# Optimization experiments

Measured on AMD Instinct MI355X. Metric: run time of the kernel, lower is better.

The kernel has to match this reference:

```python
import jax, jax.numpy as jnp
import numpy as np

ODE_UNFOLDS = 6
MOTOR_SIZE = 3
EPS = 1e-8

def _conv(x, w, b, stride):
    y = jax.lax.conv_general_dilated(x, w, (stride, stride), 'VALID',
                                     dimension_numbers=('NCHW', 'OIHW', 'NCHW'))
    return jax.nn.relu(y + b[None, :, None, None])

def _conv_head(x, w1, b1, w2, b2, w3, b3, w4, b4, w5, b5, fc_w, fc_b):
    # x: [B, T, 3, 66, 200] -> features [B, T, 128]
    B, T = x.shape[0], x.shape[1]
    h = x.reshape(B * T, *x.shape[2:])
    h = _conv(h, w1, b1, 2)  # [BT,24,31,98]
    h = _conv(h, w2, b2, 2)  # [BT,36,14,47]
    h = _conv(h, w3, b3, 2)  # [BT,48,5,22]
    h = _conv(h, w4, b4, 1)  # [BT,64,3,20]
    h = _conv(h, w5, b5, 1)  # [BT,64,1,18]
    h = h.reshape(B * T, -1)
    h = jax.nn.relu(h @ fc_w + fc_b)
    return h.reshape(B, T, -1)

def _ltc_step(inputs, v, s_mu, s_sigma, s_w, s_erev, mu, sigma, w, erev, gleak, vleak, cm):
    # inputs: [B,S], v: [B,N]
    # sensory synapse activations (constant over the ODE unfolds)
    s_act = s_w * jax.nn.sigmoid((inputs[:, :, None] - s_mu) * s_sigma)  # [B,S,N]
    w_num_s = jnp.sum(s_act * s_erev, axis=1)  # [B,N]
    w_den_s = jnp.sum(s_act, axis=1)           # [B,N]
    cm_t = cm * ODE_UNFOLDS  # cm / (elapsed=1 / ode_unfolds)
    for _ in range(ODE_UNFOLDS):
        w_act = w * jax.nn.sigmoid((v[:, :, None] - mu) * sigma)  # [B,N,N]
        w_num = jnp.sum(w_act * erev, axis=1) + w_num_s
        w_den = jnp.sum(w_act, axis=1) + w_den_s
        v = (cm_t * v + gleak * vleak + w_num) / (cm_t + gleak + w_den + EPS)
    return v[:, :MOTOR_SIZE], v

def reference(x, w1, b1, w2, b2, w3, b3, w4, b4, w5, b5, fc_w, fc_b,
              s_mu, s_sigma, s_w, s_erev, mu, sigma, w, erev, gleak, vleak, cm):
    y = _conv_head(x, w1, b1, w2, b2, w3, b3, w4, b4, w5, b5, fc_w, fc_b)  # [B,T,128]
    B, T, _ = y.shape
    N = mu.shape[0]
    v0 = jnp.zeros((B, N), dtype=y.dtype)

    def step(v, inp):
        out, v = _ltc_step(inp, v, s_mu, s_sigma, s_w, s_erev, mu, sigma, w, erev, gleak, vleak, cm)
        return v, out

    _, outs = jax.lax.scan(step, v0, jnp.swapaxes(y, 0, 1))  # outs: [T,B,3]
    return jnp.swapaxes(outs, 0, 1)  # [B,T,3]

def setup_inputs() -> dict:
    key = jax.random.key(0)
    ks = jax.random.split(key, 24)
    d = {}
    d['x'] = jax.random.normal(ks[0], (32, 16, 3, 66, 200), jnp.float32)
    shapes = [((24, 3, 5, 5), (24,)), ((36, 24, 5, 5), (36,)), ((48, 36, 5, 5), (48,)),
              ((64, 48, 3, 3), (64,)), ((64, 64, 3, 3), (64,))]
    for i, (ws, bs) in enumerate(shapes):
        d[f'w{i+1}'] = jax.random.normal(ks[1 + i], ws, jnp.float32) * 0.05
        d[f'b{i+1}'] = jnp.zeros(bs, jnp.float32)
    d['fc_w'] = jax.random.normal(ks[6], (1152, 128), jnp.float32) * 0.05
    d['fc_b'] = jnp.zeros((128,), jnp.float32)
    S, N = 128, 64
    d['s_mu'] = jax.random.normal(ks[7], (S, N), jnp.float32) * 0.3 + 0.3
    d['s_sigma'] = jax.random.uniform(ks[8], (S, N), jnp.float32, 3.0, 8.0)
    d['s_w'] = jax.random.uniform(ks[9], (S, N), jnp.float32, 0.001, 1.0)
    d['s_erev'] = jnp.sign(jax.random.normal(ks[10], (S, N), jnp.float32))
    d['mu'] = jax.random.normal(ks[11], (N, N), jnp.float32) * 0.3 + 0.3
    d['sigma'] = jax.random.uniform(ks[12], (N, N), jnp.float32, 3.0, 8.0)
    d['w'] = jax.random.uniform(ks[13], (N, N), jnp.float32, 0.001, 1.0)
    d['erev'] = jnp.sign(jax.random.normal(ks[14], (N, N), jnp.float32))
    d['gleak'] = jax.random.uniform(ks[15], (N,), jnp.float32, 0.001, 1.0)
    d['vleak'] = jax.random.uniform(ks[16], (N,), jnp.float32, -0.2, 0.2)
    d['cm'] = jax.random.uniform(ks[17], (N,), jnp.float32, 0.4, 0.6)
    return d
```

## Files before the change

### kernel.cpp

```cpp
#include <hip/hip_runtime.h>
#include <hip/hip_bf16.h>


typedef _Float16 f16;
typedef _Float16 f16x8 __attribute__((ext_vector_type(8)));
typedef _Float16 f16x4 __attribute__((ext_vector_type(4)));
typedef float    f32x4 __attribute__((ext_vector_type(4)));
typedef unsigned int u32;

static __device__ __forceinline__ float sigmoidf_fast(float x) {
    return __builtin_amdgcn_rcpf(1.0f + __expf(-x));
}

static __device__ __forceinline__ void gload_lds16(const void* g, void* l) {
    __builtin_amdgcn_global_load_lds(
        (const __attribute__((address_space(1))) void*)g,
        (__attribute__((address_space(3))) void*)l, 16, 0, 0);
}


__global__ __launch_bounds__(256)
void wpack1_kernel(const float* __restrict__ w1, f16* __restrict__ Wpk1)
{
    int idx = blockIdx.x * 256 + threadIdx.x;
    if (idx >= 32 * 136) return;
    int co = idx / 136;
    int kk = idx % 136;
    float v = 0.0f;
    if (co < 24 && kk < 120) {
        int p = kk >> 3, jj = kk & 7;
        int kh = p / 3, kwp = p % 3;
        int kws = jj >> 2, ci = jj & 3;
        int kw = 2 * kwp + kws;
        if (kw < 5 && ci < 3)
            v = w1[(((size_t)co * 3 + ci) * 5 + kh) * 5 + kw];
    }
    Wpk1[idx] = (f16)v;
}

__global__ __launch_bounds__(512)
void conv1_mfma(const float* __restrict__ x, const f16* __restrict__ Wpk1,
                const float* __restrict__ b1, f16* __restrict__ h1T)
{
    __shared__ __align__(16) f16 img[35 * 200 * 4];

    int blk  = blockIdx.x;
    int m    = blk >> 1;
    int hf   = blk & 1;
    int tid  = threadIdx.x;
    int lane = tid & 63;
    int wv   = tid >> 6;
    int col  = lane & 15;
    int row4 = lane >> 4;

    int ho_base = hf * 16;
    int r0      = 2 * ho_base;
    int nrows   = hf ? 33 : 35;
    int nho     = hf ? 15 : 16;
    int npx     = nho * 98;
    int ntile   = (npx + 15) >> 4;
    int niter   = (ntile + 7) >> 3;

    {
        const float* p0 = x + (size_t)m * 39600 + (size_t)r0 * 200;
        int n4 = (nrows * 200) >> 2;
        float4 ra[4], rb[4], rc[4];
        #pragma unroll
        for (int k = 0; k < 4; ++k) {
            int u4 = tid + k * 512;
            if (u4 < n4) {
                ra[k] = *(const float4*)(p0 + (size_t)u4 * 4);
                rb[k] = *(const float4*)(p0 + 13200 + (size_t)u4 * 4);
                rc[k] = *(const float4*)(p0 + 26400 + (size_t)u4 * 4);
            }
        }
        #pragma unroll
        for (int k = 0; k < 4; ++k) {
            int u4 = tid + k * 512;
            if (u4 < n4) {
                float4 a = ra[k], b = rb[k], c = rc[k];
                f16x8 lo = { (f16)a.x, (f16)b.x, (f16)c.x, (f16)0.0f,
                             (f16)a.y, (f16)b.y, (f16)c.y, (f16)0.0f };
                f16x8 hi = { (f16)a.z, (f16)b.z, (f16)c.z, (f16)0.0f,
                             (f16)a.w, (f16)b.w, (f16)c.w, (f16)0.0f };
                *(f16x8*)(&img[(size_t)u4 * 16])     = lo;
                *(f16x8*)(&img[(size_t)u4 * 16 + 8]) = hi;
            }
        }
    }

    f16x8 af[2][4];
    #pragma unroll
    for (int Mt = 0; Mt < 2; ++Mt)
        #pragma unroll
        for (int t = 0; t < 4; ++t)
            af[Mt][t] = *(const f16x8*)((const char*)Wpk1 +
                           (Mt * 16 + col) * 272 + t * 64 + row4 * 16);

    int rowB[4], kwpv[4];
    #pragma unroll
    for (int t = 0; t < 4; ++t) {
        int p = 4 * t + row4; if (p > 14) p = 14;
        rowB[t] = (p / 3) * 1600;
        kwpv[t] = (p % 3) * 16;
    }

    float bvv[2][4];
    #pragma unroll
    for (int Mt = 0; Mt < 2; ++Mt)
        #pragma unroll
        for (int i = 0; i < 4; ++i) {
            int co = Mt * 16 + row4 * 4 + i;
            bvv[Mt][i] = (co < 24) ? b1[co] : 0.0f;
        }

    __syncthreads();

    const char* ic = (const char*)img;
    for (int it = 0; it < niter; ++it) {
        int s = wv + it * 8;
        if (s >= ntile) continue;
        int px = s * 16 + col;
        bool pv = (px < npx);
        int pc = pv ? px : npx - 1;
        int ho_l = pc / 98;
        int wo   = pc - ho_l * 98;
        int base = ho_l * 3200 + wo * 16;

        f32x4 a0 = {0.f,0.f,0.f,0.f}, a1 = {0.f,0.f,0.f,0.f};
        #pragma unroll
        for (int t = 0; t < 4; ++t) {
            f16x8 xf = *(const f16x8*)(ic + base + rowB[t] + kwpv[t]);
            a0 = __builtin_amdgcn_mfma_f32_16x16x32_f16(af[0][t], xf, a0, 0, 0, 0);
            a1 = __builtin_amdgcn_mfma_f32_16x16x32_f16(af[1][t], xf, a1, 0, 0, 0);
        }

        if (pv) {
            int ho = ho_base + ho_l;
            size_t rowbase = ((size_t)m * 31 + ho) * 296;
            int par = (wo & 1) * 49, wh = wo >> 1;
            int j0 = (row4 & 1) * 4;
            {
                int c8 = row4 >> 1;
                f16x4 pk = { (f16)fmaxf(a0[0] + bvv[0][0], 0.0f),
                             (f16)fmaxf(a0[1] + bvv[0][1], 0.0f),
                             (f16)fmaxf(a0[2] + bvv[0][2], 0.0f),
                             (f16)fmaxf(a0[3] + bvv[0][3], 0.0f) };
                int sl = c8 * 98 + par + wh;
                *(f16x4*)(h1T + (rowbase + sl) * 8 + j0) = pk;
            }
            if (row4 < 2) {
                f16x4 pk = { (f16)fmaxf(a1[0] + bvv[1][0], 0.0f),
                             (f16)fmaxf(a1[1] + bvv[1][1], 0.0f),
                             (f16)fmaxf(a1[2] + bvv[1][2], 0.0f),
                             (f16)fmaxf(a1[3] + bvv[1][3], 0.0f) };
                int sl = 2 * 98 + par + wh;
                *(f16x4*)(h1T + (rowbase + sl) * 8 + j0) = pk;
            }
        }
    }
}

__global__ __launch_bounds__(256)
void wpack_kernel(const float* __restrict__ w2, f16* __restrict__ Wpk)
{
    int idx = blockIdx.x * 256 + threadIdx.x;
    if (idx >= 48 * 616) return;
    int co = idx / 616;
    int kk = idx % 616;
    float v = 0.0f;
    if (kk < 608 && co < 36) {
        int c = kk >> 3, j = kk & 7;
        if (c < 75) {
            int pq = c / 3, c8 = c - 3 * pq;
            int kh = pq / 5, kw = pq - 5 * kh;
            int ci = c8 * 8 + j;
            v = w2[(((size_t)co * 24 + ci) * 5 + kh) * 5 + kw];
        }
    }
    Wpk[idx] = (f16)v;
}

__global__ __launch_bounds__(256)
void wpack3_kernel(const float* __restrict__ w3, f16* __restrict__ Wpk3)
{
    int idx = blockIdx.x * 256 + threadIdx.x;
    if (idx >= 48 * 1032) return;
    int co = idx / 1032;
    int kk = idx % 1032;
    float v = 0.0f;
    if (kk < 1024) {
        int c = kk >> 3, j = kk & 7;
        int pq = c / 5, c8 = c - 5 * pq;
        if (pq < 25) {
            int kh = pq / 5, kw = pq - 5 * kh;
            int ci = c8 * 8 + j;
            if (ci < 36)
                v = w3[(((size_t)co * 36 + ci) * 5 + kh) * 5 + kw];
        }
    }
    Wpk3[idx] = (f16)v;
}

__global__ __launch_bounds__(384)
void conv2_mfma(const f16* __restrict__ h1T, const f16* __restrict__ Wpk,
                const float* __restrict__ b2, f16* __restrict__ h2f)
{
    __shared__ __align__(16) f16 img[9216 * 8];
    __shared__ u32 lutS[76];

    int m    = blockIdx.x;
    int tid  = threadIdx.x;
    int lane = tid & 63;
    int wv   = tid >> 6;
    int ct   = wv >> 1;
    int sh   = wv & 1;
    int row4 = lane >> 4;
    int col  = lane & 15;

    {
        const char* g = (const char*)(h1T + (size_t)m * 73408);
        char* l = (char*)img;
        #pragma unroll
        for (int k = 0; k < 24; ++k) {
            int u0 = wv * 64 + k * 384;
            gload_lds16(g + ((size_t)(u0 + lane)) * 16, l + (size_t)u0 * 16);
        }
    }

    if (tid < 76) {
        int c = tid; u32 v = 0;
        if (c < 75) {
            int pq = c / 3, c8 = c - 3 * pq;
            int kh = pq / 5, kw = pq - 5 * kh;
            u32 ofs = (u32)(c8 * 98 + (kw & 1) * 49 + (kw >> 1));
            v = ((u32)(kh * 4736) << 8) | ofs;
        }
        lutS[c] = v;
    }

    f16x8 af[19];
    {
        const char* wb = (const char*)Wpk + (size_t)(ct * 16 + col) * 1232 + row4 * 16;
        #pragma unroll
        for (int t = 0; t < 19; ++t)
            af[t] = *(const f16x8*)(wb + t * 64);
    }

    float bv[4];
    #pragma unroll
    for (int i = 0; i < 4; ++i) {
        int co = ct * 16 + row4 * 4 + i;
        bv[i] = (co < 36) ? b2[co] : 0.0f;
    }
    int c8o  = ct * 2 + (row4 >> 1);
    int hsel = (row4 & 1) * 4;

    __syncthreads();

    const char* ic = (const char*)img;
    for (int it = 0; it < 7; ++it) {
        int rbase[3], valid[3], hov[3], wov[3];
        #pragma unroll
        for (int si = 0; si < 3; ++si) {
            int tile = sh * 21 + it * 3 + si;
            int px   = tile * 16 + col;
            valid[si] = (px < 658);
            int pc = valid[si] ? px : 657;
            int ho = pc / 47;
            int wo = pc - 47 * ho;
            rbase[si] = ho * 9472 + wo * 16;
            hov[si] = ho; wov[si] = wo;
        }

        f32x4 acc0 = {0.f,0.f,0.f,0.f}, acc1 = {0.f,0.f,0.f,0.f}, acc2 = {0.f,0.f,0.f,0.f};
        #pragma unroll
        for (int t = 0; t < 19; ++t) {
            u32 lv   = lutS[4 * t + row4];
            int rowb = (int)(lv >> 8);
            int boff = (int)(lv & 255) << 4;
            f16x8 a = af[t];
            {
                f16x8 xf = *(const f16x8*)(ic + rbase[0] + rowb + boff);
                acc0 = __builtin_amdgcn_mfma_f32_16x16x32_f16(a, xf, acc0, 0, 0, 0);
            }
            {
                f16x8 xf = *(const f16x8*)(ic + rbase[1] + rowb + boff);
                acc1 = __builtin_amdgcn_mfma_f32_16x16x32_f16(a, xf, acc1, 0, 0, 0);
            }
            {
                f16x8 xf = *(const f16x8*)(ic + rbase[2] + rowb + boff);
                acc2 = __builtin_amdgcn_mfma_f32_16x16x32_f16(a, xf, acc2, 0, 0, 0);
            }
        }

        #pragma unroll
        for (int si = 0; si < 3; ++si) {
            f32x4 a = (si == 0) ? acc0 : (si == 1) ? acc1 : acc2;
            if (valid[si] && c8o < 5) {
                int wo = wov[si], ho = hov[si];
                f16x4 pk;
                #pragma unroll
                for (int i = 0; i < 4; ++i) pk[i] = (f16)fmaxf(a[i] + bv[i], 0.0f);
                int sl = c8o * 47 + (wo & 1) * 24 + (wo >> 1);
                *(f16x4*)(h2f + ((size_t)m * 3374 + (size_t)ho * 241 + sl) * 8 + hsel) = pk;
            }
        }
    }
}

__global__ __launch_bounds__(384)
void conv3_mfma(const f16* __restrict__ h2f, const f16* __restrict__ Wpk3,
                const float* __restrict__ b3, float* __restrict__ h3)
{
    __shared__ __align__(16) f16 Wl[6208 * 8];
    __shared__ __align__(16) f16 img[3392 * 8];
    __shared__ u32 lut[128];

    int m    = blockIdx.x;
    int tid  = threadIdx.x;
    int lane = tid & 63;
    int wv   = tid >> 6;
    int ct   = wv >> 1;
    int sh   = wv & 1;
    int row4 = lane >> 4;
    int col  = lane & 15;

    {
        const char* g = (const char*)Wpk3;
        char* l = (char*)Wl;
        #pragma unroll
        for (int k = 0; k < 17; ++k) {
            int u0 = wv * 64 + k * 384;
            if (u0 < 6208)
                gload_lds16(g + ((size_t)(u0 + lane)) * 16, l + (size_t)u0 * 16);
        }
    }
    {
        const char* g = (const char*)(h2f + (size_t)m * 3374 * 8);
        char* l = (char*)img;
        #pragma unroll
        for (int k = 0; k < 9; ++k) {
            int u0 = wv * 64 + k * 384;
            if (u0 < 3392)
                gload_lds16(g + ((size_t)(u0 + lane)) * 16, l + (size_t)u0 * 16);
        }
    }

    if (tid < 128) {
        int c  = tid;
        int pq = c / 5, c8 = c - 5 * pq;
        int kh = pq / 5, kw = pq - 5 * kh;
        lut[c] = ((u32)(kh * 3856) << 8) |
                 (u32)(c8 * 47 + (kw & 1) * 24 + (kw >> 1));
    }

    int rb[4], wo16[4], valid[4], hov[4], wov[4];
    int nsi = 4 - sh;
    #pragma unroll
    for (int si = 0; si < 4; ++si) {
        int s  = 4 * sh + si;
        int px = 16 * s + col;
        valid[si] = (si < nsi) && (px < 110);
        int pc = px < 110 ? px : 109;
        int ho = pc / 22, wo = pc - 22 * ho;
        rb[si]   = ho * 7712;
        wo16[si] = wo * 16;
        hov[si]  = ho; wov[si] = wo;
    }

    float bv[4];
    #pragma unroll
    for (int i = 0; i < 4; ++i) bv[i] = b3[ct * 16 + row4 * 4 + i];

    __syncthreads();

    int Abase = (ct * 16 + col) * 2064 + row4 * 16;
    const char* Wc = (const char*)Wl;
    const char* ic = (const char*)img;

    f32x4 a0 = {0.f,0.f,0.f,0.f}, a1 = {0.f,0.f,0.f,0.f};
    f32x4 a2 = {0.f,0.f,0.f,0.f}, a3 = {0.f,0.f,0.f,0.f};
    #pragma unroll 8
    for (int t = 0; t < 32; ++t) {
        u32 lv     = lut[4 * t + row4];
        int rowoff = (int)(lv >> 8);
        int boff   = (int)(lv & 255) << 4;
        f16x8 af = *(const f16x8*)(Wc + Abase + 64 * t);
        {
            f16x8 xf = *(const f16x8*)(ic + rb[0] + rowoff + boff + wo16[0]);
            a0 = __builtin_amdgcn_mfma_f32_16x16x32_f16(af, xf, a0, 0, 0, 0);
        }
        {
            f16x8 xf = *(const f16x8*)(ic + rb[1] + rowoff + boff + wo16[1]);
            a1 = __builtin_amdgcn_mfma_f32_16x16x32_f16(af, xf, a1, 0, 0, 0);
        }
        {
            f16x8 xf = *(const f16x8*)(ic + rb[2] + rowoff + boff + wo16[2]);
            a2 = __builtin_amdgcn_mfma_f32_16x16x32_f16(af, xf, a2, 0, 0, 0);
        }
        {
            f16x8 xf = *(const f16x8*)(ic + rb[3] + rowoff + boff + wo16[3]);
            a3 = __builtin_amdgcn_mfma_f32_16x16x32_f16(af, xf, a3, 0, 0, 0);
        }
    }

    int co0 = ct * 16 + row4 * 4;
    #pragma unroll
    for (int si = 0; si < 4; ++si) {
        if (!valid[si]) continue;
        f32x4 a = (si == 0) ? a0 : (si == 1) ? a1 : (si == 2) ? a2 : a3;
        float* op = h3 + (((size_t)m * 48 + co0) * 5 + hov[si]) * 22 + wov[si];
        #pragma unroll
        for (int i = 0; i < 4; ++i)
            op[(size_t)i * 110] = fmaxf(a[i] + bv[i], 0.0f);
    }
}

template<int CIN, int KH, int KW, int STRIDE, int CO_T, int WO_T>
__global__ __launch_bounds__(256)
void conv_tile_kernel(const float* __restrict__ in, const float* __restrict__ wt,
                      const float* __restrict__ bias, float* __restrict__ out,
                      int Cout, int Hin, int Win, int Hout, int Wout,
                      int n_cg, int n_wg, int M)
{
    constexpr int LOAD_W = (WO_T - 1) * STRIDE + KW;

    int bx = blockIdx.x;
    int cg = bx % n_cg;
    int gid = (bx / n_cg) * blockDim.x + threadIdx.x;
    int wg = gid % n_wg;
    int t  = gid / n_wg;
    int ho = t % Hout;
    int m  = t / Hout;
    if (m >= M) return;

    int wo0 = wg * WO_T;
    int co0 = cg * CO_T;

    const float* ip = in + ((size_t)(m * CIN) * Hin + (size_t)ho * STRIDE) * Win
                         + (size_t)wo0 * STRIDE;
    const float* wp = wt + (size_t)co0 * (CIN * KH * KW);

    float acc[CO_T][WO_T];
    #pragma unroll
    for (int c = 0; c < CO_T; ++c) {
        float b = bias[co0 + c];
        #pragma unroll
        for (int q = 0; q < WO_T; ++q) acc[c][q] = b;
    }

    #pragma unroll 1
    for (int ci = 0; ci < CIN; ++ci) {
        #pragma unroll
        for (int kh = 0; kh < KH; ++kh) {
            const float* row = ip + ((size_t)ci * Hin + kh) * Win;
            float xv[LOAD_W];
            #pragma unroll
            for (int l = 0; l < LOAD_W; ++l) xv[l] = row[l];
            const float* wrow = wp + (ci * KH + kh) * KW;
            #pragma unroll
            for (int c = 0; c < CO_T; ++c) {
                #pragma unroll
                for (int kw = 0; kw < KW; ++kw) {
                    float wv = wrow[c * (CIN * KH * KW) + kw];
                    #pragma unroll
                    for (int q = 0; q < WO_T; ++q)
                        acc[c][q] = fmaf(xv[q * STRIDE + kw], wv, acc[c][q]);
                }
            }
        }
    }

    #pragma unroll
    for (int c = 0; c < CO_T; ++c) {
        float* op = out + (((size_t)m * Cout + co0 + c) * Hout + ho) * Wout + wo0;
        #pragma unroll
        for (int q = 0; q < WO_T; ++q) {
            if (wo0 + q < Wout) op[q] = fmaxf(acc[c][q], 0.0f);
        }
    }
}

__global__ __launch_bounds__(256)
void fc_relu_kernel(const float* __restrict__ h, const float* __restrict__ w,
                    const float* __restrict__ b, float* __restrict__ out)
{
    __shared__ float hs[1152];
    __shared__ float part[8][32][4];
    int f   = blockIdx.x;
    int tid = threadIdx.x;
    int ks  = tid >> 5;
    int j4  = tid & 31;
    for (int k = tid; k < 1152; k += 256) hs[k] = h[(size_t)f * 1152 + k];
    __syncthreads();
    const float4* w4 = (const float4*)w;
    float4 acc = {0.f, 0.f, 0.f, 0.f};
    int k0 = ks * 144;
    #pragma unroll 4
    for (int kk = 0; kk < 144; ++kk) {
        int k = k0 + kk;
        float4 wv = w4[(size_t)k * 32 + j4];
        float hb = hs[k];
        acc.x = fmaf(wv.x, hb, acc.x);
        acc.y = fmaf(wv.y, hb, acc.y);
        acc.z = fmaf(wv.z, hb, acc.z);
        acc.w = fmaf(wv.w, hb, acc.w);
    }
    *(float4*)&part[ks][j4][0] = acc;
    __syncthreads();
    if (tid < 128) {
        int j = tid, jq = j >> 2, r = j & 3;
        float s = b[j];
        #pragma unroll
        for (int q = 0; q < 8; ++q) s += part[q][jq][r];
        out[(size_t)f * 128 + j] = fmaxf(s, 0.0f);
    }
}

__global__ __launch_bounds__(64)
void sensory_kernel(const float* __restrict__ feat,
                    const float* __restrict__ s_mu,
                    const float* __restrict__ s_sigma,
                    const float* __restrict__ s_w,
                    const float* __restrict__ s_erev,
                    float* __restrict__ wnum, float* __restrict__ wden)
{
    __shared__ float y[128];
    int bt = blockIdx.x;
    int n  = threadIdx.x;
    for (int s = n; s < 128; s += 64) y[s] = feat[bt * 128 + s];
    __syncthreads();
    float num = 0.0f, den = 0.0f;
    for (int s = 0; s < 128; ++s) {
        int o = s * 64 + n;
        float a = s_w[o] * sigmoidf_fast((y[s] - s_mu[o]) * s_sigma[o]);
        num = fmaf(a, s_erev[o], num);
        den += a;
    }
    wnum[bt * 64 + n] = num;
    wden[bt * 64 + n] = den;
}

__global__ __launch_bounds__(512)
void ltc_wave_kernel(const float* __restrict__ wnum_s,
                     const float* __restrict__ wden_s,
                     const float* __restrict__ mu, const float* __restrict__ sigma,
                     const float* __restrict__ w, const float* __restrict__ erev,
                     const float* __restrict__ gleak, const float* __restrict__ vleak,
                     const float* __restrict__ cm, float* __restrict__ out, int T)
{
    __shared__ float2 pnd[2][8][64];

    int b    = blockIdx.x;
    int tid  = threadIdx.x;
    int lane = tid & 63;
    int p    = tid >> 6;

    float musig[8], nsg[8], wvv[8], wev[8];
    #pragma unroll
    for (int ii = 0; ii < 8; ++ii) {
        int o = (8 * p + ii) * 64 + lane;
        float sg = sigma[o];
        musig[ii] = mu[o] * sg;
        nsg[ii]   = -sg;
        float wl  = w[o];
        wvv[ii]   = wl;
        wev[ii]   = wl * erev[o];
    }
    float gl   = gleak[lane];
    float glvl = gl * vleak[lane];
    float cmt  = cm[lane] * 6.0f;
    float v    = 0.0f;
    int   buf  = 0;

    for (int t = 0; t < T; ++t) {
        float ns = wnum_s[(b * T + t) * 64 + lane];
        float ds = wden_s[(b * T + t) * 64 + lane];
        #pragma unroll 1
        for (int u = 0; u < 6; ++u) {
            float num = 0.0f, den = 0.0f;
            #pragma unroll
            for (int ii = 0; ii < 8; ++ii) {
                float vi  = __shfl(v, 8 * p + ii);
                float arg = fmaf(vi, nsg[ii], musig[ii]);
                float e   = __expf(arg);
                float s   = __builtin_amdgcn_rcpf(1.0f + e);
                den = fmaf(wvv[ii], s, den);
                num = fmaf(wev[ii], s, num);
            }
            pnd[buf][p][lane] = make_float2(num, den);
            __syncthreads();
            float wn = ns, wd = ds;
            #pragma unroll
            for (int q = 0; q < 8; ++q) {
                float2 pq = pnd[buf][q][lane];
                wn += pq.x; wd += pq.y;
            }
            v = (fmaf(cmt, v, glvl) + wn) *
                __builtin_amdgcn_rcpf(cmt + gl + wd + 1e-8f);
            buf ^= 1;
        }
        if (tid < 3) out[(b * T + t) * 3 + tid] = v;
    }
}

extern "C" void kernel_launch(void* const* d_in, const int* in_sizes, int n_in,
                              void* d_out, int out_size, void* d_ws, size_t ws_size,
                              hipStream_t stream)
{
    (void)in_sizes; (void)n_in; (void)out_size; (void)ws_size;

    const float* x    = (const float*)d_in[0];
    const float* w1   = (const float*)d_in[1];
    const float* b1   = (const float*)d_in[2];
    const float* w2   = (const float*)d_in[3];
    const float* b2   = (const float*)d_in[4];
    const float* w3   = (const float*)d_in[5];
    const float* b3   = (const float*)d_in[6];
    const float* w4   = (const float*)d_in[7];
    const float* b4   = (const float*)d_in[8];
    const float* w5   = (const float*)d_in[9];
    const float* b5   = (const float*)d_in[10];
    const float* fcw  = (const float*)d_in[11];
    const float* fcb  = (const float*)d_in[12];
    const float* smu  = (const float*)d_in[13];
    const float* ssig = (const float*)d_in[14];
    const float* sw   = (const float*)d_in[15];
    const float* serv = (const float*)d_in[16];
    const float* mu   = (const float*)d_in[17];
    const float* sig  = (const float*)d_in[18];
    const float* ww   = (const float*)d_in[19];
    const float* erev = (const float*)d_in[20];
    const float* gl   = (const float*)d_in[21];
    const float* vl   = (const float*)d_in[22];
    const float* cm   = (const float*)d_in[23];
    float* out = (float*)d_out;

    const int BT = 512;

    char* wsB = (char*)d_ws;
    size_t off = 0;
    f16*   h1T  = (f16*)(wsB + off); off += (size_t)512 * 31 * 2368 * 2;
    f16*   Wpk  = (f16*)(wsB + off); off += 65536;
    f16*   h2f  = (f16*)(wsB + off); off += (size_t)512 * 3374 * 16;
    f16*   Wpk3 = (f16*)(wsB + off); off += 48 * 1032 * 2;
    f16*   Wpk1 = (f16*)(wsB + off); off += 32 * 136 * 2;
    float* h3   = (float*)(wsB + off); off += (size_t)512 * 48 * 5 * 22 * 4;
    float* h4   = (float*)(wsB + off); off += (size_t)512 * 64 * 3 * 20 * 4;
    float* h5   = (float*)(wsB + off); off += (size_t)512 * 64 * 18 * 4;
    float* feat = (float*)(wsB + off); off += (size_t)BT * 128 * 4;
    float* wnum = (float*)(wsB + off); off += (size_t)BT * 64 * 4;
    float* wden = (float*)(wsB + off); off += (size_t)BT * 64 * 4;

    wpack1_kernel<<<(32 * 136 + 255) / 256, 256, 0, stream>>>(w1, Wpk1);
    wpack_kernel<<<(48 * 616 + 255) / 256, 256, 0, stream>>>(w2, Wpk);
    wpack3_kernel<<<(48 * 1032 + 255) / 256, 256, 0, stream>>>(w3, Wpk3);

    conv1_mfma<<<1024, 512, 0, stream>>>(x, Wpk1, b1, h1T);
    conv2_mfma<<<512, 384, 0, stream>>>(h1T, Wpk, b2, h2f);
    conv3_mfma<<<512, 384, 0, stream>>>(h2f, Wpk3, b3, h3);

    {
        int n_cg = 16, n_wg = 5;
        int sp_threads = BT * 3 * n_wg;
        int grid = (sp_threads + 255) / 256 * n_cg;
        conv_tile_kernel<48, 3, 3, 1, 4, 4><<<grid, 256, 0, stream>>>(
            h3, w4, b4, h4, 64, 5, 22, 3, 20, n_cg, n_wg, BT);
    }
    {
        int n_cg = 16, n_wg = 6;
        int sp_threads = BT * 1 * n_wg;
        int grid = (sp_threads + 255) / 256 * n_cg;
        conv_tile_kernel<64, 3, 3, 1, 4, 3><<<grid, 256, 0, stream>>>(
            h4, w5, b5, h5, 64, 3, 20, 1, 18, n_cg, n_wg, BT);
    }
    fc_relu_kernel<<<512, 256, 0, stream>>>(h5, fcw, fcb, feat);
    sensory_kernel<<<BT, 64, 0, stream>>>(feat, smu, ssig, sw, serv, wnum, wden);
    ltc_wave_kernel<<<32, 512, 0, stream>>>(wnum, wden, mu, sig, ww, erev,
                                            gl, vl, cm, out, 16);
}
```

Baseline: 248.9 us.

## Fuse conv3 through sensory stage into one per-frame kernel; merge weight packers

Fuses conv3, conv4, conv5, the FC layer and the sensory synapse reduction into a single per-frame block. Intermediate activations stay in LDS instead of round-tripping through global memory. The three weight-pack kernels are also merged into one launch to cut launch overhead. In exchange, each block of conv4, conv5 and FC work is small and reads weights directly from global memory with limited parallelism, and LDS use grows, which may limit occupancy.

```diff
diff --git a/kernel.cpp b/kernel.cpp
--- a/kernel.cpp
+++ b/kernel.cpp
@@ -20,22 +20,57 @@
 
 
 __global__ __launch_bounds__(256)
-void wpack1_kernel(const float* __restrict__ w1, f16* __restrict__ Wpk1)
+void wpack_all(const float* __restrict__ w1, f16* __restrict__ Wpk1,
+               const float* __restrict__ w2, f16* __restrict__ Wpk,
+               const float* __restrict__ w3, f16* __restrict__ Wpk3)
 {
-    int idx = blockIdx.x * 256 + threadIdx.x;
-    if (idx >= 32 * 136) return;
-    int co = idx / 136;
-    int kk = idx % 136;
-    float v = 0.0f;
-    if (co < 24 && kk < 120) {
-        int p = kk >> 3, jj = kk & 7;
-        int kh = p / 3, kwp = p % 3;
-        int kws = jj >> 2, ci = jj & 3;
-        int kw = 2 * kwp + kws;
-        if (kw < 5 && ci < 3)
-            v = w1[(((size_t)co * 3 + ci) * 5 + kh) * 5 + kw];
-    }
-    Wpk1[idx] = (f16)v;
+    int bx = blockIdx.x;
+    if (bx < 17) {
+        int idx = bx * 256 + threadIdx.x;
+        if (idx >= 32 * 136) return;
+        int co = idx / 136, kk = idx % 136;
+        float v = 0.0f;
+        if (co < 24 && kk < 120) {
+            int p = kk >> 3, jj = kk & 7;
+            int kh = p / 3, kwp = p % 3;
+            int kws = jj >> 2, ci = jj & 3;
+            int kw = 2 * kwp + kws;
+            if (kw < 5 && ci < 3)
+                v = w1[(((size_t)co * 3 + ci) * 5 + kh) * 5 + kw];
+        }
+        Wpk1[idx] = (f16)v;
+    } else if (bx < 133) {
+        int idx = (bx - 17) * 256 + threadIdx.x;
+        if (idx >= 48 * 616) return;
+        int co = idx / 616, kk = idx % 616;
+        float v = 0.0f;
+        if (kk < 608 && co < 36) {
+            int c = kk >> 3, j = kk & 7;
+            if (c < 75) {
+                int pq = c / 3, c8 = c - 3 * pq;
+                int kh = pq / 5, kw = pq - 5 * kh;
+                int ci = c8 * 8 + j;
+                v = w2[(((size_t)co * 24 + ci) * 5 + kh) * 5 + kw];
+            }
+        }
+        Wpk[idx] = (f16)v;
+    } else {
+        int idx = (bx - 133) * 256 + threadIdx.x;
+        if (idx >= 48 * 1032) return;
+        int co = idx / 1032, kk = idx % 1032;
+        float v = 0.0f;
+        if (kk < 1024) {
+            int c = kk >> 3, j = kk & 7;
+            int pq = c / 5, c8 = c - 5 * pq;
+            if (pq < 25) {
+                int kh = pq / 5, kw = pq - 5 * kh;
+                int ci = c8 * 8 + j;
+                if (ci < 36)
+                    v = w3[(((size_t)co * 36 + ci) * 5 + kh) * 5 + kw];
+            }
+        }
+        Wpk3[idx] = (f16)v;
+    }
 }
 
 __global__ __launch_bounds__(512)
@@ -161,47 +196,6 @@
     }
 }
 
-__global__ __launch_bounds__(256)
-void wpack_kernel(const float* __restrict__ w2, f16* __restrict__ Wpk)
-{
-    int idx = blockIdx.x * 256 + threadIdx.x;
-    if (idx >= 48 * 616) return;
-    int co = idx / 616;
-    int kk = idx % 616;
-    float v = 0.0f;
-    if (kk < 608 && co < 36) {
-        int c = kk >> 3, j = kk & 7;
-        if (c < 75) {
-            int pq = c / 3, c8 = c - 3 * pq;
-            int kh = pq / 5, kw = pq - 5 * kh;
-            int ci = c8 * 8 + j;
-            v = w2[(((size_t)co * 24 + ci) * 5 + kh) * 5 + kw];
-        }
-    }
-    Wpk[idx] = (f16)v;
-}
-
-__global__ __launch_bounds__(256)
-void wpack3_kernel(const float* __restrict__ w3, f16* __restrict__ Wpk3)
-{
-    int idx = blockIdx.x * 256 + threadIdx.x;
-    if (idx >= 48 * 1032) return;
-    int co = idx / 1032;
-    int kk = idx % 1032;
-    float v = 0.0f;
-    if (kk < 1024) {
-        int c = kk >> 3, j = kk & 7;
-        int pq = c / 5, c8 = c - 5 * pq;
-        if (pq < 25) {
-            int kh = pq / 5, kw = pq - 5 * kh;
-            int ci = c8 * 8 + j;
-            if (ci < 36)
-                v = w3[(((size_t)co * 36 + ci) * 5 + kh) * 5 + kw];
-        }
-    }
-    Wpk3[idx] = (f16)v;
-}
-
 __global__ __launch_bounds__(384)
 void conv2_mfma(const f16* __restrict__ h1T, const f16* __restrict__ Wpk,
                 const float* __restrict__ b2, f16* __restrict__ h2f)
@@ -310,12 +304,26 @@
 }
 
 __global__ __launch_bounds__(384)
-void conv3_mfma(const f16* __restrict__ h2f, const f16* __restrict__ Wpk3,
-                const float* __restrict__ b3, float* __restrict__ h3)
+void tail_fused(const f16* __restrict__ h2f, const f16* __restrict__ Wpk3,
+                const float* __restrict__ b3,
+                const float* __restrict__ w4g, const float* __restrict__ b4,
+                const float* __restrict__ w5g, const float* __restrict__ b5,
+                const float* __restrict__ fcw, const float* __restrict__ fcb,
+                const float* __restrict__ smu, const float* __restrict__ ssig,
+                const float* __restrict__ swt, const float* __restrict__ serv,
+                float* __restrict__ wnum, float* __restrict__ wden)
 {
-    __shared__ __align__(16) f16 Wl[6208 * 8];
-    __shared__ __align__(16) f16 img[3392 * 8];
+    __shared__ __align__(16) char smem[153600];
     __shared__ u32 lut[128];
+
+    f16* Wl    = (f16*)smem;
+    f16* img   = (f16*)(smem + 99328);
+    float* h3L = (float*)smem;
+    float* h4L = (float*)(smem + 21120);
+    float* h5L = (float*)(smem + 36480);
+    float* featL = (float*)(smem + 41088);
+    float* pFC = (float*)(smem + 41600);
+    float2* pSN = (float2*)(smem + 43136);
 
     int m    = blockIdx.x;
     int tid  = threadIdx.x;
@@ -355,13 +363,13 @@
                  (u32)(c8 * 47 + (kw & 1) * 24 + (kw >> 1));
     }
 
-    int rb[4], wo16[4], valid[4], hov[4], wov[4];
+    int rb[4], wo16[4], valid3[4], hov[4], wov[4];
     int nsi = 4 - sh;
     #pragma unroll
     for (int si = 0; si < 4; ++si) {
         int s  = 4 * sh + si;
         int px = 16 * s + col;
-        valid[si] = (si < nsi) && (px < 110);
+        valid3[si] = (si < nsi) && (px < 110);
         int pc = px < 110 ? px : 109;
         int ho = pc / 22, wo = pc - 22 * ho;
         rb[si]   = ho * 7712;
@@ -386,160 +394,166 @@
         u32 lv     = lut[4 * t + row4];
         int rowoff = (int)(lv >> 8);
         int boff   = (int)(lv & 255) << 4;
-        f16x8 af = *(const f16x8*)(Wc + Abase + 64 * t);
+        f16x8 afr = *(const f16x8*)(Wc + Abase + 64 * t);
         {
             f16x8 xf = *(const f16x8*)(ic + rb[0] + rowoff + boff + wo16[0]);
-            a0 = __builtin_amdgcn_mfma_f32_16x16x32_f16(af, xf, a0, 0, 0, 0);
+            a0 = __builtin_amdgcn_mfma_f32_16x16x32_f16(afr, xf, a0, 0, 0, 0);
         }
         {
             f16x8 xf = *(const f16x8*)(ic + rb[1] + rowoff + boff + wo16[1]);
-            a1 = __builtin_amdgcn_mfma_f32_16x16x32_f16(af, xf, a1, 0, 0, 0);
+            a1 = __builtin_amdgcn_mfma_f32_16x16x32_f16(afr, xf, a1, 0, 0, 0);
         }
         {
             f16x8 xf = *(const f16x8*)(ic + rb[2] + rowoff + boff + wo16[2]);
-            a2 = __builtin_amdgcn_mfma_f32_16x16x32_f16(af, xf, a2, 0, 0, 0);
+            a2 = __builtin_amdgcn_mfma_f32_16x16x32_f16(afr, xf, a2, 0, 0, 0);
         }
         {
             f16x8 xf = *(const f16x8*)(ic + rb[3] + rowoff + boff + wo16[3]);
-            a3 = __builtin_amdgcn_mfma_f32_16x16x32_f16(af, xf, a3, 0, 0, 0);
-        }
-    }
-
-    int co0 = ct * 16 + row4 * 4;
-    #pragma unroll
-    for (int si = 0; si < 4; ++si) {
-        if (!valid[si]) continue;
-        f32x4 a = (si == 0) ? a0 : (si == 1) ? a1 : (si == 2) ? a2 : a3;
-        float* op = h3 + (((size_t)m * 48 + co0) * 5 + hov[si]) * 22 + wov[si];
-        #pragma unroll
-        for (int i = 0; i < 4; ++i)
-            op[(size_t)i * 110] = fmaxf(a[i] + bv[i], 0.0f);
-    }
-}
-
-template<int CIN, int KH, int KW, int STRIDE, int CO_T, int WO_T>
-__global__ __launch_bounds__(256)
-void conv_tile_kernel(const float* __restrict__ in, const float* __restrict__ wt,
-                      const float* __restrict__ bias, float* __restrict__ out,
-                      int Cout, int Hin, int Win, int Hout, int Wout,
-                      int n_cg, int n_wg, int M)
-{
-    constexpr int LOAD_W = (WO_T - 1) * STRIDE + KW;
-
-    int bx = blockIdx.x;
-    int cg = bx % n_cg;
-    int gid = (bx / n_cg) * blockDim.x + threadIdx.x;
-    int wg = gid % n_wg;
-    int t  = gid / n_wg;
-    int ho = t % Hout;
-    int m  = t / Hout;
-    if (m >= M) return;
-
-    int wo0 = wg * WO_T;
-    int co0 = cg * CO_T;
-
-    const float* ip = in + ((size_t)(m * CIN) * Hin + (size_t)ho * STRIDE) * Win
-                         + (size_t)wo0 * STRIDE;
-    const float* wp = wt + (size_t)co0 * (CIN * KH * KW);
-
-    float acc[CO_T][WO_T];
-    #pragma unroll
-    for (int c = 0; c < CO_T; ++c) {
-        float b = bias[co0 + c];
-        #pragma unroll
-        for (int q = 0; q < WO_T; ++q) acc[c][q] = b;
-    }
-
-    #pragma unroll 1
-    for (int ci = 0; ci < CIN; ++ci) {
-        #pragma unroll
-        for (int kh = 0; kh < KH; ++kh) {
-            const float* row = ip + ((size_t)ci * Hin + kh) * Win;
-            float xv[LOAD_W];
+            a3 = __builtin_amdgcn_mfma_f32_16x16x32_f16(afr, xf, a3, 0, 0, 0);
+        }
+    }
+
+    __syncthreads();
+
+    {
+        int co0 = ct * 16 + row4 * 4;
+        #pragma unroll
+        for (int si = 0; si < 4; ++si) {
+            if (!valid3[si]) continue;
+            f32x4 a = (si == 0) ? a0 : (si == 1) ? a1 : (si == 2) ? a2 : a3;
+            float* op = h3L + (size_t)co0 * 110 + hov[si] * 22 + wov[si];
             #pragma unroll
-            for (int l = 0; l < LOAD_W; ++l) xv[l] = row[l];
-            const float* wrow = wp + (ci * KH + kh) * KW;
+            for (int i = 0; i < 4; ++i)
+                op[(size_t)i * 110] = fmaxf(a[i] + bv[i], 0.0f);
+        }
+    }
+    __syncthreads();
+
+    {
+        int px = lane;
+        bool pxv = px < 60;
+        int r4 = px / 20, c4 = px - 20 * (px / 20);
+        int nco = (wv < 4) ? 11 : 10;
+        float acc4[11];
+        #pragma unroll
+        for (int k = 0; k < 11; ++k)
+            acc4[k] = (k < nco) ? b4[wv + 6 * k] : 0.0f;
+        if (pxv) {
+            for (int cc = 0; cc < 48; ++cc) {
+                #pragma unroll
+                for (int kh = 0; kh < 3; ++kh) {
+                    float i0 = h3L[cc * 110 + (r4 + kh) * 22 + c4];
+                    float i1 = h3L[cc * 110 + (r4 + kh) * 22 + c4 + 1];
+                    float i2 = h3L[cc * 110 + (r4 + kh) * 22 + c4 + 2];
+                    #pragma unroll
+                    for (int k = 0; k < 11; ++k) {
+                        if (k < nco) {
+                            const float* wr = w4g + (((size_t)(wv + 6 * k) * 48 + cc) * 3 + kh) * 3;
+                            acc4[k] = fmaf(i0, wr[0], acc4[k]);
+                            acc4[k] = fmaf(i1, wr[1], acc4[k]);
+                            acc4[k] = fmaf(i2, wr[2], acc4[k]);
+                        }
+                    }
+                }
+            }
+        }
+        __syncthreads();
+        if (pxv) {
             #pragma unroll
-            for (int c = 0; c < CO_T; ++c) {
+            for (int k = 0; k < 11; ++k)
+                if (k < nco)
+                    h4L[(wv + 6 * k) * 60 + px] = fmaxf(acc4[k], 0.0f);
+        }
+    }
+    __syncthreads();
+
+    {
+        int q  = lane / 18;
+        int wo = lane - 18 * q;
+        bool lv = (lane < 54);
+        int c0 = (q == 0) ? 0 : (q == 1) ? 22 : 43;
+        int c1 = (q == 0) ? 22 : (q == 1) ? 43 : 64;
+        int nco = (wv < 4) ? 11 : 10;
+        float acc5[11];
+        #pragma unroll
+        for (int k = 0; k < 11; ++k) acc5[k] = 0.0f;
+        if (lv) {
+            for (int cc = c0; cc < c1; ++cc) {
+                float in9[9];
                 #pragma unroll
-                for (int kw = 0; kw < KW; ++kw) {
-                    float wv = wrow[c * (CIN * KH * KW) + kw];
+                for (int kh = 0; kh < 3; ++kh)
                     #pragma unroll
-                    for (int q = 0; q < WO_T; ++q)
-                        acc[c][q] = fmaf(xv[q * STRIDE + kw], wv, acc[c][q]);
+                    for (int kw = 0; kw < 3; ++kw)
+                        in9[kh * 3 + kw] = h4L[cc * 60 + kh * 20 + wo + kw];
+                #pragma unroll
+                for (int k = 0; k < 11; ++k) {
+                    if (k < nco) {
+                        const float* wr = w5g + ((size_t)(wv + 6 * k) * 64 + cc) * 9;
+                        #pragma unroll
+                        for (int e = 0; e < 9; ++e)
+                            acc5[k] = fmaf(in9[e], wr[e], acc5[k]);
+                    }
                 }
             }
         }
-    }
-
-    #pragma unroll
-    for (int c = 0; c < CO_T; ++c) {
-        float* op = out + (((size_t)m * Cout + co0 + c) * Hout + ho) * Wout + wo0;
-        #pragma unroll
-        for (int q = 0; q < WO_T; ++q) {
-            if (wo0 + q < Wout) op[q] = fmaxf(acc[c][q], 0.0f);
-        }
-    }
-}
-
-__global__ __launch_bounds__(256)
-void fc_relu_kernel(const float* __restrict__ h, const float* __restrict__ w,
-                    const float* __restrict__ b, float* __restrict__ out)
-{
-    __shared__ float hs[1152];
-    __shared__ float part[8][32][4];
-    int f   = blockIdx.x;
-    int tid = threadIdx.x;
-    int ks  = tid >> 5;
-    int j4  = tid & 31;
-    for (int k = tid; k < 1152; k += 256) hs[k] = h[(size_t)f * 1152 + k];
-    __syncthreads();
-    const float4* w4 = (const float4*)w;
-    float4 acc = {0.f, 0.f, 0.f, 0.f};
-    int k0 = ks * 144;
-    #pragma unroll 4
-    for (int kk = 0; kk < 144; ++kk) {
-        int k = k0 + kk;
-        float4 wv = w4[(size_t)k * 32 + j4];
-        float hb = hs[k];
-        acc.x = fmaf(wv.x, hb, acc.x);
-        acc.y = fmaf(wv.y, hb, acc.y);
-        acc.z = fmaf(wv.z, hb, acc.z);
-        acc.w = fmaf(wv.w, hb, acc.w);
-    }
-    *(float4*)&part[ks][j4][0] = acc;
+        #pragma unroll
+        for (int k = 0; k < 11; ++k) {
+            float v1 = __shfl(acc5[k], lane + 18);
+            float v2 = __shfl(acc5[k], lane + 36);
+            acc5[k] = acc5[k] + v1 + v2;
+        }
+        if (lv && q == 0) {
+            #pragma unroll
+            for (int k = 0; k < 11; ++k)
+                if (k < nco)
+                    h5L[(wv + 6 * k) * 18 + wo] = fmaxf(acc5[k] + b5[wv + 6 * k], 0.0f);
+        }
+    }
+    __syncthreads();
+
+    {
+        int j = tid & 127;
+        int q = tid >> 7;
+        float a = 0.0f;
+        int k0 = q * 384;
+        for (int kk = 0; kk < 384; ++kk) {
+            int k = k0 + kk;
+            a = fmaf(h5L[k], fcw[(size_t)k * 128 + j], a);
+        }
+        pFC[q * 128 + j] = a;
+    }
     __syncthreads();
     if (tid < 128) {
-        int j = tid, jq = j >> 2, r = j & 3;
-        float s = b[j];
-        #pragma unroll
-        for (int q = 0; q < 8; ++q) s += part[q][jq][r];
-        out[(size_t)f * 128 + j] = fmaxf(s, 0.0f);
-    }
-}
-
-__global__ __launch_bounds__(64)
-void sensory_kernel(const float* __restrict__ feat,
-                    const float* __restrict__ s_mu,
-                    const float* __restrict__ s_sigma,
-                    const float* __restrict__ s_w,
-                    const float* __restrict__ s_erev,
-                    float* __restrict__ wnum, float* __restrict__ wden)
-{
-    __shared__ float y[128];
-    int bt = blockIdx.x;
-    int n  = threadIdx.x;
-    for (int s = n; s < 128; s += 64) y[s] = feat[bt * 128 + s];
-    __syncthreads();
-    float num = 0.0f, den = 0.0f;
-    for (int s = 0; s < 128; ++s) {
-        int o = s * 64 + n;
-        float a = s_w[o] * sigmoidf_fast((y[s] - s_mu[o]) * s_sigma[o]);
-        num = fmaf(a, s_erev[o], num);
-        den += a;
-    }
-    wnum[bt * 64 + n] = num;
-    wden[bt * 64 + n] = den;
+        float s = fcb[tid] + pFC[tid] + pFC[128 + tid] + pFC[256 + tid];
+        featL[tid] = fmaxf(s, 0.0f);
+    }
+    __syncthreads();
+
+    {
+        int n = tid & 63;
+        int q = tid >> 6;
+        int s0 = q * 22;
+        int s1 = s0 + 22; if (s1 > 128) s1 = 128;
+        float num = 0.0f, den = 0.0f;
+        for (int s = s0; s < s1; ++s) {
+            int o = s * 64 + n;
+            float a = swt[o] * sigmoidf_fast((featL[s] - smu[o]) * ssig[o]);
+            num = fmaf(a, serv[o], num);
+            den += a;
+        }
+        pSN[q * 64 + n] = make_float2(num, den);
+    }
+    __syncthreads();
+    if (tid < 64) {
+        float num = 0.0f, den = 0.0f;
+        #pragma unroll
+        for (int q = 0; q < 6; ++q) {
+            float2 p = pSN[q * 64 + tid];
+            num += p.x; den += p.y;
+        }
+        wnum[(size_t)m * 64 + tid] = num;
+        wden[(size_t)m * 64 + tid] = den;
+    }
 }
 
 __global__ __launch_bounds__(512)
@@ -646,37 +660,15 @@
     f16*   h2f  = (f16*)(wsB + off); off += (size_t)512 * 3374 * 16;
     f16*   Wpk3 = (f16*)(wsB + off); off += 48 * 1032 * 2;
     f16*   Wpk1 = (f16*)(wsB + off); off += 32 * 136 * 2;
-    float* h3   = (float*)(wsB + off); off += (size_t)512 * 48 * 5 * 22 * 4;
-    float* h4   = (float*)(wsB + off); off += (size_t)512 * 64 * 3 * 20 * 4;
-    float* h5   = (float*)(wsB + off); off += (size_t)512 * 64 * 18 * 4;
-    float* feat = (float*)(wsB + off); off += (size_t)BT * 128 * 4;
     float* wnum = (float*)(wsB + off); off += (size_t)BT * 64 * 4;
     float* wden = (float*)(wsB + off); off += (size_t)BT * 64 * 4;
 
-    wpack1_kernel<<<(32 * 136 + 255) / 256, 256, 0, stream>>>(w1, Wpk1);
-    wpack_kernel<<<(48 * 616 + 255) / 256, 256, 0, stream>>>(w2, Wpk);
-    wpack3_kernel<<<(48 * 1032 + 255) / 256, 256, 0, stream>>>(w3, Wpk3);
-
+    wpack_all<<<327, 256, 0, stream>>>(w1, Wpk1, w2, Wpk, w3, Wpk3);
     conv1_mfma<<<1024, 512, 0, stream>>>(x, Wpk1, b1, h1T);
     conv2_mfma<<<512, 384, 0, stream>>>(h1T, Wpk, b2, h2f);
-    conv3_mfma<<<512, 384, 0, stream>>>(h2f, Wpk3, b3, h3);
-
-    {
-        int n_cg = 16, n_wg = 5;
-        int sp_threads = BT * 3 * n_wg;
-        int grid = (sp_threads + 255) / 256 * n_cg;
-        conv_tile_kernel<48, 3, 3, 1, 4, 4><<<grid, 256, 0, stream>>>(
-            h3, w4, b4, h4, 64, 5, 22, 3, 20, n_cg, n_wg, BT);
-    }
-    {
-        int n_cg = 16, n_wg = 6;
-        int sp_threads = BT * 1 * n_wg;
-        int grid = (sp_threads + 255) / 256 * n_cg;
-        conv_tile_kernel<64, 3, 3, 1, 4, 3><<<grid, 256, 0, stream>>>(
-            h4, w5, b5, h5, 64, 3, 20, 1, 18, n_cg, n_wg, BT);
-    }
-    fc_relu_kernel<<<512, 256, 0, stream>>>(h5, fcw, fcb, feat);
-    sensory_kernel<<<BT, 64, 0, stream>>>(feat, smu, ssig, sw, serv, wnum, wden);
+    tail_fused<<<512, 384, 0, stream>>>(h2f, Wpk3, b3, w4, b4, w5, b5,
+                                        fcw, fcb, smu, ssig, sw, serv,
+                                        wnum, wden);
     ltc_wave_kernel<<<32, 512, 0, stream>>>(wnum, wden, mu, sig, ww, erev,
                                             gl, vl, cm, out, 16);
 }
```

New measurement: 353.6 us. 42.0% more time.
